# Kernel optimization log

Measured on AMD Instinct MI355X. Metric: run time of the kernel, lower is better.

The kernel has to match this reference:

```python
import jax, jax.numpy as jnp
import numpy as np


def setup_inputs() -> dict:
    key = jax.random.key(0)
    ks = jax.random.split(key, 6)
    B, S, AD, QD, A = 64, 2048, 1024, 1024, 1024
    scale = 0.02
    return {
        "input": jax.random.normal(ks[0], (B, QD), dtype=jnp.float32),
        "context": jax.random.normal(ks[1], (B, S, AD), dtype=jnp.float32),
        "W_pre": jax.random.normal(ks[2], (A, AD), dtype=jnp.float32) * scale,
        "b_pre": jax.random.normal(ks[3], (A,), dtype=jnp.float32) * scale,
        "W_q": jax.random.normal(ks[4], (A, QD), dtype=jnp.float32) * scale,
        "v": jax.random.normal(ks[5], (A,), dtype=jnp.float32) * scale,
    }


def reference(input, context, W_pre, b_pre, W_q, v):
    # precompute = linear_pre(context): [B, S, A]
    precompute = jnp.einsum("bsd,ad->bsa", context, W_pre) + b_pre
    # targetT = linear_q(input): [B, A], broadcast over sourceL
    targetT = jnp.einsum("bq,aq->ba", input, W_q)
    tmp = jnp.tanh(precompute + targetT[:, None, :])  # [B, S, A]
    energy = jnp.einsum("bsa,a->bs", tmp, v)          # linear_v, [B, S]
    score = jax.nn.softmax(energy, axis=1)             # softmax over sourceL
    weightedContext = jnp.einsum("bs,bsd->bd", score, context)
    return weightedContext, score, precompute
```

## Files before the change

kernel.cpp:

```cpp
#include <hip/hip_runtime.h>
#include <hip/hip_bf16.h>

#define BB   64
#define SS   2048
#define MM   (BB*SS)
#define NN   1024
#define KK   1024

typedef short bf16x8s __attribute__((ext_vector_type(8)));
typedef float f32x4   __attribute__((ext_vector_type(4)));

__device__ __forceinline__ short f2bf(float f) {
    union { __hip_bfloat16 h; short s; } u;
    u.h = __float2bfloat16(f);
    return u.s;
}

__device__ __forceinline__ bf16x8s cvt8(float4 a, float4 b) {
    bf16x8s r;
    r[0] = f2bf(a.x); r[1] = f2bf(a.y); r[2] = f2bf(a.z); r[3] = f2bf(a.w);
    r[4] = f2bf(b.x); r[5] = f2bf(b.y); r[6] = f2bf(b.z); r[7] = f2bf(b.w);
    return r;
}

__device__ __forceinline__ float tanh_fast(float x) {
    x = fminf(8.0f, fmaxf(-8.0f, x));
    float e = __expf(2.0f * x);
    return 1.0f - 2.0f * __builtin_amdgcn_rcpf(e + 1.0f);
}

__device__ __forceinline__ void load_lds16(const void* g, void* l) {
    __builtin_amdgcn_global_load_lds(
        (const __attribute__((address_space(1))) unsigned int*)g,
        (__attribute__((address_space(3))) unsigned int*)l,
        16, 0, 0);
}

__global__ void cvt_bf16_kernel(const float* __restrict__ src,
                                __hip_bfloat16* __restrict__ dst, int n8) {
    int i = blockIdx.x * blockDim.x + threadIdx.x;
    const int stride = gridDim.x * blockDim.x;
    const float4* s4 = (const float4*)src;
    bf16x8s* d8 = (bf16x8s*)dst;
    for (; i < n8; i += stride) {
        d8[i] = cvt8(s4[i * 2], s4[i * 2 + 1]);
    }
}

__global__ void targetT_kernel(const float* __restrict__ input,
                               const float* __restrict__ W_q,
                               float* __restrict__ tgt) {
    __shared__ float inp[KK];
    const int t = threadIdx.x;
    const int b = blockIdx.x;
    const float* inRow = input + (size_t)b * KK;
    for (int i = t; i < KK; i += 256) inp[i] = inRow[i];
    __syncthreads();
    const int w = t >> 6, lane = t & 63;
    const int nbase = blockIdx.y * 256 + w * 64;
    for (int i = 0; i < 64; i++) {
        const int n = nbase + i;
        const float* wq = W_q + (size_t)n * KK;
        float a = 0.f;
        #pragma unroll
        for (int j = 0; j < 16; j++) a += wq[lane + 64 * j] * inp[lane + 64 * j];
        #pragma unroll
        for (int o = 32; o; o >>= 1) a += __shfl_xor(a, o);
        if (lane == 0) tgt[(size_t)b * NN + n] = a;
    }
}

__global__ __launch_bounds__(512, 2) void gemm8_kernel(
    const __hip_bfloat16* __restrict__ ctxb,
    const __hip_bfloat16* __restrict__ wpb,
    const float* __restrict__ bpre,
    const float* __restrict__ tgt,
    const float* __restrict__ vvec,
    float* __restrict__ pre,
    float* __restrict__ energy4,
    int row0)
{
    __shared__ __align__(16) char lds[131072];

    const int nwg  = gridDim.x;
    const int orig = blockIdx.x;
    const int swz  = (orig & 7) * (nwg >> 3) + (orig >> 3);
    const int mTile = swz >> 2;
    const int nTile = swz & 3;
    const int blockM = mTile * 256;
    const int blockN = nTile * 256;

    const int t = threadIdx.x, w = t >> 6, lane = t & 63;
    const int wm = w >> 2, wn = w & 3;
    const int l15 = lane & 15;

    const int r0  = t >> 3;
    const int lc0 = ((t & 7) * 16) ^ ((r0 & 7) << 4);
    const char* aSrc = (const char*)ctxb + (size_t)(blockM + r0) * 2048 + lc0;
    const char* bSrc = (const char*)wpb  + (size_t)(blockN + r0) * 2048 + lc0;

#define STAGE_AF(buf, T) do { \
    load_lds16(aSrc +          (T)*128, &lds[(buf)*32768 +         w*1024]); \
    load_lds16(aSrc + 131072 + (T)*128, &lds[(buf)*32768 +  8192 + w*1024]); \
    load_lds16(aSrc + 262144 + (T)*128, &lds[(buf)*32768 + 16384 + w*1024]); \
    load_lds16(aSrc + 393216 + (T)*128, &lds[(buf)*32768 + 24576 + w*1024]); \
} while(0)
#define STAGE_BF(buf, T) do { \
    load_lds16(bSrc +          (T)*128, &lds[65536 + (buf)*32768 +         w*1024]); \
    load_lds16(bSrc + 131072 + (T)*128, &lds[65536 + (buf)*32768 +  8192 + w*1024]); \
    load_lds16(bSrc + 262144 + (T)*128, &lds[65536 + (buf)*32768 + 16384 + w*1024]); \
    load_lds16(bSrc + 393216 + (T)*128, &lds[65536 + (buf)*32768 + 24576 + w*1024]); \
} while(0)

    const int c16 = (lane >> 4) * 16;
    const int xo  = (lane & 7) << 4;
    const int bk0 = c16 ^ xo;
    const int bk1 = (64 + c16) ^ xo;
    const int aBase = wm * 16384 + l15 * 128;
    const int bBase = 65536 + wn * 8192 + l15 * 128;

    bf16x8s curA[4][2], Bf[4][2];

#define READ_A(buf, mbase) do { \
    _Pragma("unroll") \
    for (int mf = 0; mf < 4; mf++) { \
        curA[mf][0] = *(const bf16x8s*)&lds[(buf)*32768 + aBase + ((mbase)+mf)*2048 + bk0]; \
        curA[mf][1] = *(const bf16x8s*)&lds[(buf)*32768 + aBase + ((mbase)+mf)*2048 + bk1]; \
    } } while(0)
#define READ_B(buf) do { \
    _Pragma("unroll") \
    for (int nf = 0; nf < 4; nf++) { \
        Bf[nf][0] = *(const bf16x8s*)&lds[(buf)*32768 + bBase + (nf)*2048 + bk0]; \
        Bf[nf][1] = *(const bf16x8s*)&lds[(buf)*32768 + bBase + (nf)*2048 + bk1]; \
    } } while(0)

    f32x4 acc[8][4];
    #pragma unroll
    for (int m = 0; m < 8; m++)
        #pragma unroll
        for (int n = 0; n < 4; n++)
            acc[m][n] = f32x4{0.f, 0.f, 0.f, 0.f};

#define MFMA_H(mbase) do { \
    _Pragma("unroll") \
    for (int ks = 0; ks < 2; ks++) \
        _Pragma("unroll") \
        for (int mf = 0; mf < 4; mf++) \
            _Pragma("unroll") \
            for (int nf = 0; nf < 4; nf++) \
                acc[(mbase)+mf][nf] = __builtin_amdgcn_mfma_f32_16x16x32_bf16( \
                    curA[mf][ks], Bf[nf][ks], acc[(mbase)+mf][nf], 0, 0, 0); \
} while(0)

#define BAR() do { __builtin_amdgcn_sched_barrier(0); \
    __builtin_amdgcn_s_barrier(); \
    __builtin_amdgcn_sched_barrier(0); } while(0)
#define VMCNT(n) asm volatile("s_waitcnt vmcnt(" #n ")")

    STAGE_AF(0, 0);
    STAGE_BF(0, 0);
    STAGE_BF(1, 1);
    VMCNT(4);
    BAR();

    #pragma unroll 1
    for (int i = 0; i < 7; i++) {
        const int To = 2 * i + 1, Te2 = 2 * i + 2, To2 = 2 * i + 3;
        READ_A(0, 0); READ_B(0);
        STAGE_AF(1, To);
        MFMA_H(0);
        BAR();
        READ_A(0, 4);
        STAGE_BF(0, Te2);
        MFMA_H(4);
        VMCNT(4);
        BAR();
        READ_A(1, 0); READ_B(1);
        STAGE_AF(0, Te2);
        MFMA_H(0);
        BAR();
        READ_A(1, 4);
        STAGE_BF(1, To2);
        MFMA_H(4);
        VMCNT(4);
        BAR();
    }

    READ_A(0, 0); READ_B(0);
    STAGE_AF(1, 15);
    MFMA_H(0);
    BAR();
    READ_A(0, 4);
    MFMA_H(4);
    VMCNT(0);
    BAR();
    READ_A(1, 0); READ_B(1);
    MFMA_H(0);
    BAR();
    READ_A(1, 4);
    MFMA_H(4);

    const int bIdx = (row0 + blockM) >> 11;
    float bp[4], tq[4], vv[4];
    #pragma unroll
    for (int nf = 0; nf < 4; nf++) {
        const int col = blockN + wn * 64 + nf * 16 + l15;
        bp[nf] = bpre[col];
        tq[nf] = tgt[(size_t)bIdx * NN + col];
        vv[nf] = vvec[col];
    }
    const int gr0 = blockM + wm * 128 + ((lane >> 4) << 2);
    const int colBase = blockN + wn * 64 + l15;
    float* epart = energy4 + (size_t)nTile * MM;

    #pragma unroll
    for (int mf = 0; mf < 8; mf++) {
        #pragma unroll
        for (int j = 0; j < 4; j++) {
            const size_t rg = (size_t)row0 + gr0 + mf * 16 + j;
            float* prow = pre + rg * NN + colBase;
            float e = 0.f;
            #pragma unroll
            for (int nf = 0; nf < 4; nf++) {
                const float p = acc[mf][nf][j] + bp[nf];
                prow[nf * 16] = p;
                e += tanh_fast(p + tq[nf]) * vv[nf];
            }
            e += __shfl_xor(e, 1);
            e += __shfl_xor(e, 2);
            e += __shfl_xor(e, 4);
            e += __shfl_xor(e, 8);
            if (l15 == 0) epart[rg] = e;
        }
    }
#undef STAGE_AF
#undef STAGE_BF
#undef READ_A
#undef READ_B
#undef MFMA_H
#undef BAR
#undef VMCNT
}

__global__ __launch_bounds__(256, 2) void gemm_energy_kernel(
    const float* __restrict__ ctx, const float* __restrict__ wpre,
    const float* __restrict__ bpre, const float* __restrict__ tgt,
    const float* __restrict__ vvec, float* __restrict__ pre,
    float* __restrict__ energy4)
{
    __shared__ __align__(16) float As[128 * 32];
    __shared__ __align__(16) float Bs[128 * 32];

    const int orig = blockIdx.x;
    const int swz  = (orig & 7) * 1024 + (orig >> 3);
    const int mTile = swz >> 3;
    const int nTile = swz & 7;
    const size_t blockM = (size_t)mTile * 128;
    const int    blockN = nTile * 128;

    const int t = threadIdx.x, w = t >> 6, lane = t & 63;

    size_t aoff[4], boff[4];
    #pragma unroll
    for (int i = 0; i < 4; i++) {
        const int bb    = i * 4096 + w * 1024 + lane * 16;
        const int row   = bb >> 7;
        const int physc = bb & 127;
        const int logc  = physc ^ ((row & 7) << 4);
        aoff[i] = (blockM + (size_t)row) * (KK * 4) + logc;
        boff[i] = ((size_t)(blockN + row)) * (KK * 4) + logc;
    }
    const char* ctxB  = (const char*)ctx;
    const char* wpreB = (const char*)wpre;

    const int wm = (w >> 1) * 64, wn = (w & 1) * 64;

    int fa0[4], fa1[4], fb0[4], fb1[4];
    const int c0 = (lane >> 4) * 32;
    #pragma unroll
    for (int m = 0; m < 4; m++) {
        const int rA = wm + m * 16 + (lane & 15);
        const int sA = (rA & 7) << 4;
        fa0[m] = rA * 128 + (c0 ^ sA);
        fa1[m] = rA * 128 + ((c0 + 16) ^ sA);
        const int rB = wn + m * 16 + (lane & 15);
        const int sB = (rB & 7) << 4;
        fb0[m] = rB * 128 + (c0 ^ sB);
        fb1[m] = rB * 128 + ((c0 + 16) ^ sB);
    }

    f32x4 acc[4][4];
    #pragma unroll
    for (int m = 0; m < 4; m++)
        #pragma unroll
        for (int n = 0; n < 4; n++)
            acc[m][n] = f32x4{0.f, 0.f, 0.f, 0.f};

    for (int kt = 0; kt < KK / 32; kt++) {
        __syncthreads();
        #pragma unroll
        for (int i = 0; i < 4; i++) {
            load_lds16(ctxB  + aoff[i] + (size_t)kt * 128,
                       (char*)As + i * 4096 + w * 1024);
            load_lds16(wpreB + boff[i] + (size_t)kt * 128,
                       (char*)Bs + i * 4096 + w * 1024);
        }
        __syncthreads();

        bf16x8s af[4], bfr[4];
        #pragma unroll
        for (int m = 0; m < 4; m++) {
            float4 x0 = *(const float4*)((const char*)As + fa0[m]);
            float4 x1 = *(const float4*)((const char*)As + fa1[m]);
            af[m] = cvt8(x0, x1);
            float4 y0 = *(const float4*)((const char*)Bs + fb0[m]);
            float4 y1 = *(const float4*)((const char*)Bs + fb1[m]);
            bfr[m] = cvt8(y0, y1);
        }
        #pragma unroll
        for (int m = 0; m < 4; m++)
            #pragma unroll
            for (int n = 0; n < 4; n++)
                acc[m][n] = __builtin_amdgcn_mfma_f32_16x16x32_bf16(
                    af[m], bfr[n], acc[m][n], 0, 0, 0);
    }

    const int bIdx = (int)(blockM >> 11);
    float bp[4], tq[4], vv[4];
    #pragma unroll
    for (int n = 0; n < 4; n++) {
        const int col = blockN + wn + n * 16 + (lane & 15);
        bp[n] = bpre[col];
        tq[n] = tgt[(size_t)bIdx * NN + col];
        vv[n] = vvec[col];
    }
    const int colBase = blockN + wn + (lane & 15);

    #pragma unroll
    for (int m = 0; m < 4; m++) {
        const size_t rbase = blockM + wm + m * 16 + ((lane >> 4) << 2);
        #pragma unroll
        for (int j = 0; j < 4; j++) {
            const size_t rg = rbase + j;
            float* prow = pre + rg * NN + colBase;
            float e = 0.f;
            #pragma unroll
            for (int n = 0; n < 4; n++) {
                const float p = acc[m][n][j] + bp[n];
                prow[n * 16] = p;
                e += tanh_fast(p + tq[n]) * vv[n];
            }
            e += __shfl_xor(e, 1);
            e += __shfl_xor(e, 2);
            e += __shfl_xor(e, 4);
            e += __shfl_xor(e, 8);
            if ((lane & 15) == 0) atomicAdd(&energy4[rg], e);
        }
    }
}

__global__ void softmax_kernel(const float* __restrict__ energy4,
                               float* __restrict__ score) {
    const int b = blockIdx.x, t = threadIdx.x;
    const int w = t >> 6, lane = t & 63;
    const size_t base = (size_t)b * SS;
    float x[8] = {0.f, 0.f, 0.f, 0.f, 0.f, 0.f, 0.f, 0.f};
    #pragma unroll
    for (int p = 0; p < 4; p++) {
        const float4* e4 = (const float4*)(energy4 + (size_t)p * MM + base);
        float4 v0 = e4[t * 2], v1 = e4[t * 2 + 1];
        x[0] += v0.x; x[1] += v0.y; x[2] += v0.z; x[3] += v0.w;
        x[4] += v1.x; x[5] += v1.y; x[6] += v1.z; x[7] += v1.w;
    }

    float mx = x[0];
    #pragma unroll
    for (int i = 1; i < 8; i++) mx = fmaxf(mx, x[i]);
    #pragma unroll
    for (int o = 32; o; o >>= 1) mx = fmaxf(mx, __shfl_xor(mx, o));
    __shared__ float rmax[4], rsum[4];
    if (lane == 0) rmax[w] = mx;
    __syncthreads();
    mx = fmaxf(fmaxf(rmax[0], rmax[1]), fmaxf(rmax[2], rmax[3]));

    float s = 0.f;
    #pragma unroll
    for (int i = 0; i < 8; i++) { x[i] = __expf(x[i] - mx); s += x[i]; }
    #pragma unroll
    for (int o = 32; o; o >>= 1) s += __shfl_xor(s, o);
    if (lane == 0) rsum[w] = s;
    __syncthreads();
    s = rsum[0] + rsum[1] + rsum[2] + rsum[3];
    const float inv = 1.0f / s;

    float* sc = score + base + t * 8;
    #pragma unroll
    for (int i = 0; i < 8; i++) sc[i] = x[i] * inv;
}

__global__ void wctx_bf16_kernel(const __hip_bfloat16* __restrict__ ctxb,
                                 const float* __restrict__ score,
                                 float* __restrict__ wc) {
    const int b = blockIdx.x, scnk = blockIdx.y, t = threadIdx.x;
    __shared__ float ss[256];
    ss[t] = score[(size_t)b * SS + scnk * 256 + t];
    __syncthreads();
    const ushort4* cr = (const ushort4*)(ctxb + ((size_t)b * SS + (size_t)scnk * 256) * KK) + t;
    float4 a = {0.f, 0.f, 0.f, 0.f};
    #pragma unroll 4
    for (int s = 0; s < 256; s++) {
        const ushort4 c = cr[(size_t)s * 256];
        const float wgt = ss[s];
        a.x += wgt * __uint_as_float((unsigned)c.x << 16);
        a.y += wgt * __uint_as_float((unsigned)c.y << 16);
        a.z += wgt * __uint_as_float((unsigned)c.z << 16);
        a.w += wgt * __uint_as_float((unsigned)c.w << 16);
    }
    float* o = wc + (size_t)b * KK + t * 4;
    atomicAdd(o + 0, a.x);
    atomicAdd(o + 1, a.y);
    atomicAdd(o + 2, a.z);
    atomicAdd(o + 3, a.w);
}

__global__ void wctx_kernel(const float* __restrict__ ctx,
                            const float* __restrict__ score,
                            float* __restrict__ wc) {
    const int b = blockIdx.x, scnk = blockIdx.y, t = threadIdx.x;
    __shared__ float ss[256];
    ss[t] = score[(size_t)b * SS + scnk * 256 + t];
    __syncthreads();
    const float4* cr = (const float4*)(ctx + ((size_t)b * SS + (size_t)scnk * 256) * KK) + t;
    float4 a = {0.f, 0.f, 0.f, 0.f};
    #pragma unroll 4
    for (int s = 0; s < 256; s++) {
        const float4 c = cr[(size_t)s * 256];
        const float wgt = ss[s];
        a.x += wgt * c.x; a.y += wgt * c.y; a.z += wgt * c.z; a.w += wgt * c.w;
    }
    float* o = wc + (size_t)b * KK + t * 4;
    atomicAdd(o + 0, a.x);
    atomicAdd(o + 1, a.y);
    atomicAdd(o + 2, a.z);
    atomicAdd(o + 3, a.w);
}

extern "C" void kernel_launch(void* const* d_in, const int* in_sizes, int n_in,
                              void* d_out, int out_size, void* d_ws, size_t ws_size,
                              hipStream_t stream) {
    const float* input = (const float*)d_in[0];
    const float* ctx   = (const float*)d_in[1];
    const float* W_pre = (const float*)d_in[2];
    const float* b_pre = (const float*)d_in[3];
    const float* W_q   = (const float*)d_in[4];
    const float* v     = (const float*)d_in[5];

    float* out   = (float*)d_out;
    float* wc    = out;
    float* score = out + 65536;
    float* pre   = out + 65536 + 131072;

    float* tgt     = (float*)d_ws;
    float* energy4 = (float*)((char*)d_ws + 262144);
    __hip_bfloat16* wpb  = (__hip_bfloat16*)((char*)d_ws + 262144 + 2097152);
    __hip_bfloat16* ctxb = (__hip_bfloat16*)((char*)d_ws + 262144 + 2097152 + 2097152);

    long long avail = (long long)ws_size - 262144LL - 2097152LL - 2097152LL;
    long long cr = avail > 0 ? (avail / (KK * 2)) : 0;
    cr &= ~511LL;
    int chunk_rows = (int)(cr > MM ? MM : cr);

    hipMemsetAsync(wc, 0, (size_t)BB * KK * sizeof(float), stream);

    targetT_kernel<<<dim3(BB, 4), 256, 0, stream>>>(input, W_q, tgt);

    if (chunk_rows >= 512) {
        cvt_bf16_kernel<<<512, 256, 0, stream>>>(W_pre, wpb, NN * KK / 8);
        for (int r0 = 0; r0 < MM; r0 += chunk_rows) {
            const int rows = (MM - r0) < chunk_rows ? (MM - r0) : chunk_rows;
            const int n8 = rows * KK / 8;
            const int cgrid = (n8 + 255) / 256 > 4096 ? 4096 : (n8 + 255) / 256;
            cvt_bf16_kernel<<<cgrid, 256, 0, stream>>>(
                ctx + (size_t)r0 * KK, ctxb, n8);
            gemm8_kernel<<<dim3((rows / 256) * 4), 512, 0, stream>>>(
                ctxb, wpb, b_pre, tgt, v, pre, energy4, r0);
        }
    } else {
        hipMemsetAsync(energy4, 0, (size_t)4 * MM * sizeof(float), stream);
        gemm_energy_kernel<<<dim3((MM / 128) * (NN / 128)), 256, 0, stream>>>(
            ctx, W_pre, b_pre, tgt, v, pre, energy4);
    }

    softmax_kernel<<<dim3(BB), 256, 0, stream>>>(energy4, score);

    if (chunk_rows >= MM) {
        wctx_bf16_kernel<<<dim3(BB, 8), 256, 0, stream>>>(ctxb, score, wc);
    } else {
        wctx_kernel<<<dim3(BB, 8), 256, 0, stream>>>(ctx, score, wc);
    }
}
```

Baseline: 590.6 us.

## Triple-buffer A tiles in LDS with two-tile-ahead prefetch

Reworks the GEMM main loop so A tiles use a three-slot LDS ring and are prefetched two K-steps ahead, while B stays double-buffered. The two-iteration unrolled body becomes a single loop with rotating buffer offsets. The goal is to hide more global-load latency behind the MFMA work. LDS use grows from 128KB to 160KB per block. That likely cuts occupancy from the 2 blocks per CU requested in launch_bounds to 1 on a 160KB-LDS CU.

After: 593.5 us. No clear change (+0.5%).

```diff
diff --git a/kernel.cpp b/kernel.cpp
--- a/kernel.cpp
+++ b/kernel.cpp
@@ -80,7 +80,7 @@
     float* __restrict__ energy4,
     int row0)
 {
-    __shared__ __align__(16) char lds[131072];
+    __shared__ __align__(16) char lds[163840];
 
     const int nwg  = gridDim.x;
     const int orig = blockIdx.x;
@@ -100,16 +100,16 @@
     const char* bSrc = (const char*)wpb  + (size_t)(blockN + r0) * 2048 + lc0;
 
 #define STAGE_AF(buf, T) do { \
-    load_lds16(aSrc +          (T)*128, &lds[(buf)*32768 +         w*1024]); \
-    load_lds16(aSrc + 131072 + (T)*128, &lds[(buf)*32768 +  8192 + w*1024]); \
-    load_lds16(aSrc + 262144 + (T)*128, &lds[(buf)*32768 + 16384 + w*1024]); \
-    load_lds16(aSrc + 393216 + (T)*128, &lds[(buf)*32768 + 24576 + w*1024]); \
+    load_lds16(aSrc +          (T)*128, &lds[(buf) +         w*1024]); \
+    load_lds16(aSrc + 131072 + (T)*128, &lds[(buf) +  8192 + w*1024]); \
+    load_lds16(aSrc + 262144 + (T)*128, &lds[(buf) + 16384 + w*1024]); \
+    load_lds16(aSrc + 393216 + (T)*128, &lds[(buf) + 24576 + w*1024]); \
 } while(0)
 #define STAGE_BF(buf, T) do { \
-    load_lds16(bSrc +          (T)*128, &lds[65536 + (buf)*32768 +         w*1024]); \
-    load_lds16(bSrc + 131072 + (T)*128, &lds[65536 + (buf)*32768 +  8192 + w*1024]); \
-    load_lds16(bSrc + 262144 + (T)*128, &lds[65536 + (buf)*32768 + 16384 + w*1024]); \
-    load_lds16(bSrc + 393216 + (T)*128, &lds[65536 + (buf)*32768 + 24576 + w*1024]); \
+    load_lds16(bSrc +          (T)*128, &lds[(buf) +         w*1024]); \
+    load_lds16(bSrc + 131072 + (T)*128, &lds[(buf) +  8192 + w*1024]); \
+    load_lds16(bSrc + 262144 + (T)*128, &lds[(buf) + 16384 + w*1024]); \
+    load_lds16(bSrc + 393216 + (T)*128, &lds[(buf) + 24576 + w*1024]); \
 } while(0)
 
     const int c16 = (lane >> 4) * 16;
@@ -117,21 +117,21 @@
     const int bk0 = c16 ^ xo;
     const int bk1 = (64 + c16) ^ xo;
     const int aBase = wm * 16384 + l15 * 128;
-    const int bBase = 65536 + wn * 8192 + l15 * 128;
+    const int bBase = wn * 8192 + l15 * 128;
 
     bf16x8s curA[4][2], Bf[4][2];
 
 #define READ_A(buf, mbase) do { \
     _Pragma("unroll") \
     for (int mf = 0; mf < 4; mf++) { \
-        curA[mf][0] = *(const bf16x8s*)&lds[(buf)*32768 + aBase + ((mbase)+mf)*2048 + bk0]; \
-        curA[mf][1] = *(const bf16x8s*)&lds[(buf)*32768 + aBase + ((mbase)+mf)*2048 + bk1]; \
+        curA[mf][0] = *(const bf16x8s*)&lds[(buf) + aBase + ((mbase)+mf)*2048 + bk0]; \
+        curA[mf][1] = *(const bf16x8s*)&lds[(buf) + aBase + ((mbase)+mf)*2048 + bk1]; \
     } } while(0)
 #define READ_B(buf) do { \
     _Pragma("unroll") \
     for (int nf = 0; nf < 4; nf++) { \
-        Bf[nf][0] = *(const bf16x8s*)&lds[(buf)*32768 + bBase + (nf)*2048 + bk0]; \
-        Bf[nf][1] = *(const bf16x8s*)&lds[(buf)*32768 + bBase + (nf)*2048 + bk1]; \
+        Bf[nf][0] = *(const bf16x8s*)&lds[(buf) + bBase + (nf)*2048 + bk0]; \
+        Bf[nf][1] = *(const bf16x8s*)&lds[(buf) + bBase + (nf)*2048 + bk1]; \
     } } while(0)
 
     f32x4 acc[8][4];
@@ -158,46 +158,45 @@
 #define VMCNT(n) asm volatile("s_waitcnt vmcnt(" #n ")")
 
     STAGE_AF(0, 0);
-    STAGE_BF(0, 0);
-    STAGE_BF(1, 1);
-    VMCNT(4);
+    STAGE_BF(98304, 0);
+    STAGE_AF(32768, 1);
+    STAGE_BF(131072, 1);
+    VMCNT(8);
     BAR();
 
+    int aCur = 0, aNxt2 = 65536;
+    int bCur = 98304, bNxt = 131072;
+
     #pragma unroll 1
-    for (int i = 0; i < 7; i++) {
-        const int To = 2 * i + 1, Te2 = 2 * i + 2, To2 = 2 * i + 3;
-        READ_A(0, 0); READ_B(0);
-        STAGE_AF(1, To);
+    for (int kt = 0; kt < 14; ++kt) {
+        READ_A(aCur, 0); READ_B(bCur);
+        STAGE_AF(aNxt2, kt + 2);
         MFMA_H(0);
         BAR();
-        READ_A(0, 4);
-        STAGE_BF(0, Te2);
+        READ_A(aCur, 4);
+        STAGE_BF(bCur, kt + 2);
         MFMA_H(4);
-        VMCNT(4);
+        VMCNT(8);
         BAR();
-        READ_A(1, 0); READ_B(1);
-        STAGE_AF(0, Te2);
-        MFMA_H(0);
-        BAR();
-        READ_A(1, 4);
-        STAGE_BF(1, To2);
-        MFMA_H(4);
-        VMCNT(4);
-        BAR();
-    }
-
-    READ_A(0, 0); READ_B(0);
-    STAGE_AF(1, 15);
+        aCur  += 32768; if (aCur  > 65536) aCur  = 0;
+        aNxt2 += 32768; if (aNxt2 > 65536) aNxt2 = 0;
+        int tb = bCur; bCur = bNxt; bNxt = tb;
+    }
+
+    READ_A(aCur, 0); READ_B(bCur);
     MFMA_H(0);
     BAR();
-    READ_A(0, 4);
+    READ_A(aCur, 4);
     MFMA_H(4);
     VMCNT(0);
     BAR();
-    READ_A(1, 0); READ_B(1);
+    aCur += 32768; if (aCur > 65536) aCur = 0;
+    { int tb = bCur; bCur = bNxt; bNxt = tb; }
+
+    READ_A(aCur, 0); READ_B(bCur);
     MFMA_H(0);
     BAR();
-    READ_A(1, 4);
+    READ_A(aCur, 4);
     MFMA_H(4);
 
     const int bIdx = (row0 + blockM) >> 11;
```
